# Kernel tuning notes

Hardware: AMD Instinct MI355X
Metric: run time of the kernel (lower is better)

## Reference

```python
import jax, jax.numpy as jnp
import numpy as np


def setup_inputs() -> dict:
    key = jax.random.key(0)
    B, F1, F2 = 1024, 32, 16
    X = jax.random.normal(key, (B, F1, F2), dtype=jnp.float32)
    return {"X": X}


def reference(X) -> jnp.ndarray:
    # Flatten feature dims: [B, ele]
    B = X.shape[0]
    ele = X.shape[1] * X.shape[2]
    x = X.reshape(B, ele)
    # Upper-triangular pair indices (i outer, j inner, j >= i) — matches the
    # torch double loop's row-major enumeration of pairs.
    ii, jj = jnp.triu_indices(ele)  # each [ele*(ele+1)/2]
    # Pairwise products via gather + elementwise mul (avoids full [B,ele,ele] outer)
    out = x[:, ii] * x[:, jj]  # [B, npairs]
    return out[:, :, None]  # [B, npairs, 1]
```

## Files before the change

### kernel.cpp

```cpp
#include <hip/hip_runtime.h>
#include <hip/hip_bf16.h>


#define ELE 512
#define NPAIRS 131328
#define GROUPS 32832
#define BPB 8
#define GPB 4104

typedef float f4 __attribute__((ext_vector_type(4)));

__global__ __launch_bounds__(256) void pairmul4_kernel(
    const float* __restrict__ X, float* __restrict__ out) {
    const int bid = blockIdx.x;
    const int b = bid >> 3;
    const int c = bid & 7;

    const float* __restrict__ xb = X + (size_t)b * ELE;
    f4* __restrict__ ob = (f4*)(out + (size_t)b * NPAIRS);

    __shared__ __align__(16) float xs4[4][516];
    const int t = threadIdx.x;
    #pragma unroll
    for (int cc = 0; cc < 4; ++cc) {
        xs4[cc][t] = xb[t + cc];
        const int m1 = t + 256;
        xs4[cc][m1] = (m1 + cc < ELE) ? xb[m1 + cc] : 0.0f;
    }
    if (t < 16) xs4[t & 3][512 + (t >> 2)] = 0.0f;
    __syncthreads();

    const float x511 = xs4[0][511];
    const float lastsq = x511 * x511;
    const float x2 = xs4[0][2];
    const float g255sq = x2 * x2;

    const int glo = c * GPB;
    const int ghi = glo + GPB;

    for (int g = glo + t; g < ghi; g += 256) {
        const int p = g << 2;
        const float s = sqrtf((float)(1050625 - 8 * p));
        int i = (int)((1025.0f - s) * 0.5f);
        i = min(max(i, 0), 511);
        int onext = ((i + 1) * (1024 - i)) >> 1;
        i += (p >= onext);
        onext = ((i + 1) * (1024 - i)) >> 1;
        i += (p >= onext);
        int ocur = (i * (1025 - i)) >> 1;
        i -= (p < ocur);

        const int o0 = (i * (1025 - i)) >> 1;
        const int L  = ELE - i;
        const int o1 = o0 + L;

        const int j0 = i + (p - o0);
        int j1 = j0 + 1 - L;
        j1 = max(j1, 0);

        const f4 r0 = ((const f4*)xs4[j0 & 3])[j0 >> 2];
        const f4 r1 = ((const f4*)xs4[j1 & 3])[j1 >> 2];
        const float xi0 = xs4[0][i];
        const float xi1 = xs4[0][i + 1];

        const int split = o1 - p;
        f4 v;
        v.x = (0 < split) ? xi0 * r0.x : xi1 * r1.x;
        v.y = (1 < split) ? xi0 * r0.y : xi1 * r1.y;
        v.z = (2 < split) ? xi0 * r0.z : xi1 * r1.z;
        v.w = (3 < split) ? xi0 * r0.w : xi1 * r1.w;
        v.w = (g == 255) ? g255sq : v.w;
        v.w = (g == GROUPS - 1) ? lastsq : v.w;
        ob[g] = v;
    }
}

extern "C" void kernel_launch(void* const* d_in, const int* in_sizes, int n_in,
                              void* d_out, int out_size, void* d_ws, size_t ws_size,
                              hipStream_t stream) {
    const float* X = (const float*)d_in[0];
    float* out = (float*)d_out;

    const int B = in_sizes[0] / ELE;
    dim3 grid(B * BPB);
    dim3 block(256);
    pairmul4_kernel<<<grid, block, 0, stream>>>(X, out);
}
```

Before: 110.6 us.

## Precompute packed pair-index table and read it in the main kernel

Adds a small kernel that computes, for each output group, the row index i, the column index j0 and the split point, and packs them into one uint32 in workspace. The main kernel then reads this table instead of running the sqrt-based triangular index inversion and its corrections for every group, and uses a fixed 16-iteration unrolled loop with a short tail. This trades per-thread ALU work for an extra launch and a 128KB table read that the 8192 blocks share and that should stay in cache. The kernel is store-bound, so the ALU saving may not matter much. The original kernel remains as a fallback when no workspace is provided.

Result: no change. 112.0 us (+1.3%).

```diff
diff --git a/kernel.cpp b/kernel.cpp
--- a/kernel.cpp
+++ b/kernel.cpp
@@ -1,5 +1,6 @@
 #include <hip/hip_runtime.h>
 #include <hip/hip_bf16.h>
+#include <stdint.h>
 
 
 #define ELE 512
@@ -10,8 +11,50 @@
 
 typedef float f4 __attribute__((ext_vector_type(4)));
 
-__global__ __launch_bounds__(256) void pairmul4_kernel(
-    const float* __restrict__ X, float* __restrict__ out) {
+__global__ __launch_bounds__(256) void build_tab(uint32_t* __restrict__ tab) {
+    const int g = blockIdx.x * 256 + threadIdx.x;
+    if (g >= GROUPS) return;
+    const int p = g << 2;
+    float s = sqrtf((float)(1050625 - 8 * p));
+    int i = (int)((1025.0f - s) * 0.5f);
+    i = min(max(i, 0), 511);
+    while ((((i + 1) * (1024 - i)) >> 1) <= p) ++i;
+    while (((i * (1025 - i)) >> 1) > p) --i;
+    const int o0 = (i * (1025 - i)) >> 1;
+    const int o1 = o0 + (ELE - i);
+    const int j0 = i + (p - o0);
+    const int split = min(o1 - p, 4);
+    tab[g] = (uint32_t)i | ((uint32_t)j0 << 9) | ((uint32_t)(split - 1) << 18);
+}
+
+__device__ __forceinline__ f4 group_val(
+    int g, const uint32_t* __restrict__ tab,
+    const float (*xs4)[516], float g255sq, float lastsq) {
+    const uint32_t u = tab[g];
+    const int i     = u & 511;
+    const int j0    = (u >> 9) & 511;
+    const int split = ((u >> 18) & 3) + 1;
+    int j1 = j0 + i - 511;
+    j1 = max(j1, 0);
+
+    const f4 r0 = ((const f4*)xs4[j0 & 3])[j0 >> 2];
+    const f4 r1 = ((const f4*)xs4[j1 & 3])[j1 >> 2];
+    const float xi0 = xs4[0][i];
+    const float xi1 = xs4[0][i + 1];
+
+    f4 v;
+    v.x = xi0 * r0.x;
+    v.y = (1 < split) ? xi0 * r0.y : xi1 * r1.y;
+    v.z = (2 < split) ? xi0 * r0.z : xi1 * r1.z;
+    v.w = (3 < split) ? xi0 * r0.w : xi1 * r1.w;
+    v.w = (g == 255) ? g255sq : v.w;
+    v.w = (g == GROUPS - 1) ? lastsq : v.w;
+    return v;
+}
+
+__global__ __launch_bounds__(256) void pairmul4_tab_kernel(
+    const float* __restrict__ X, float* __restrict__ out,
+    const uint32_t* __restrict__ tab) {
     const int bid = blockIdx.x;
     const int b = bid >> 3;
     const int c = bid & 7;
@@ -36,8 +79,41 @@
     const float g255sq = x2 * x2;
 
     const int glo = c * GPB;
+
+    #pragma unroll 4
+    for (int k = 0; k < 16; ++k) {
+        const int g = glo + t + (k << 8);
+        ob[g] = group_val(g, tab, xs4, g255sq, lastsq);
+    }
+    if (t < 8) {
+        const int g = glo + 4096 + t;
+        ob[g] = group_val(g, tab, xs4, g255sq, lastsq);
+    }
+}
+
+__global__ __launch_bounds__(256) void pairmul4_kernel(
+    const float* __restrict__ X, float* __restrict__ out) {
+    const int bid = blockIdx.x;
+    const int b = bid >> 3;
+    const int c = bid & 7;
+    const float* __restrict__ xb = X + (size_t)b * ELE;
+    f4* __restrict__ ob = (f4*)(out + (size_t)b * NPAIRS);
+    __shared__ __align__(16) float xs4[4][516];
+    const int t = threadIdx.x;
+    #pragma unroll
+    for (int cc = 0; cc < 4; ++cc) {
+        xs4[cc][t] = xb[t + cc];
+        const int m1 = t + 256;
+        xs4[cc][m1] = (m1 + cc < ELE) ? xb[m1 + cc] : 0.0f;
+    }
+    if (t < 16) xs4[t & 3][512 + (t >> 2)] = 0.0f;
+    __syncthreads();
+    const float x511 = xs4[0][511];
+    const float lastsq = x511 * x511;
+    const float x2 = xs4[0][2];
+    const float g255sq = x2 * x2;
+    const int glo = c * GPB;
     const int ghi = glo + GPB;
-
     for (int g = glo + t; g < ghi; g += 256) {
         const int p = g << 2;
         const float s = sqrtf((float)(1050625 - 8 * p));
@@ -49,20 +125,16 @@
         i += (p >= onext);
         int ocur = (i * (1025 - i)) >> 1;
         i -= (p < ocur);
-
         const int o0 = (i * (1025 - i)) >> 1;
         const int L  = ELE - i;
         const int o1 = o0 + L;
-
         const int j0 = i + (p - o0);
         int j1 = j0 + 1 - L;
         j1 = max(j1, 0);
-
         const f4 r0 = ((const f4*)xs4[j0 & 3])[j0 >> 2];
         const f4 r1 = ((const f4*)xs4[j1 & 3])[j1 >> 2];
         const float xi0 = xs4[0][i];
         const float xi1 = xs4[0][i + 1];
-
         const int split = o1 - p;
         f4 v;
         v.x = (0 < split) ? xi0 * r0.x : xi1 * r1.x;
@@ -80,9 +152,13 @@
                               hipStream_t stream) {
     const float* X = (const float*)d_in[0];
     float* out = (float*)d_out;
+    const int B = in_sizes[0] / ELE;
 
-    const int B = in_sizes[0] / ELE;
-    dim3 grid(B * BPB);
-    dim3 block(256);
-    pairmul4_kernel<<<grid, block, 0, stream>>>(X, out);
+    if (ws_size >= (size_t)GROUPS * sizeof(uint32_t)) {
+        uint32_t* tab = (uint32_t*)d_ws;
+        build_tab<<<(GROUPS + 255) / 256, 256, 0, stream>>>(tab);
+        pairmul4_tab_kernel<<<dim3(B * BPB), dim3(256), 0, stream>>>(X, out, tab);
+    } else {
+        pairmul4_kernel<<<dim3(B * BPB), dim3(256), 0, stream>>>(X, out);
+    }
 }
```
